# Optimization experiments

Measured on AMD Instinct MI355X. Metric: run time of the kernel, lower is better.

The kernel has to match this reference:

```python
import jax, jax.numpy as jnp
import numpy as np

GAMMA = 0.99
CLIP_VALUE = 5.0
B, T = 4096, 4096


def setup_inputs() -> dict:
    key = jax.random.key(0)
    k1, k2, k3, k4 = jax.random.split(key, 4)
    return {
        "log_probs": jax.random.normal(k1, (B, T), dtype=jnp.float32),
        "logits": jax.random.normal(k2, (B, T), dtype=jnp.float32),
        "weight": jax.random.uniform(k3, (B, T), dtype=jnp.float32),
        "baselines": jax.random.normal(k4, (B, T), dtype=jnp.float32),
    }


def _discounted_reverse_cumsum(wr):
    # wr: [B, T]. c[t] = wr[t] + GAMMA * c[t+1]  (reverse linear recurrence)
    def step(carry, x):
        c = x + GAMMA * carry
        return c, c
    # scan over time, reversed; xs shape [T, B]
    _, cs = jax.lax.scan(step, jnp.zeros(wr.shape[0], wr.dtype), wr.T, reverse=True)
    return cs.T  # [B, T]


def reference(log_probs, logits, weight, baselines):
    rewards = jax.nn.log_sigmoid(logits)                    # [B, T]
    cumulative_rewards = _discounted_reverse_cumsum(weight * rewards)
    advantages = cumulative_rewards - baselines
    advantages = advantages - advantages.mean(axis=0)       # center over batch
    advantages = jnp.clip(advantages, -CLIP_VALUE, CLIP_VALUE)
    generator_objective = (advantages * log_probs).sum(axis=1)  # [B]
    return generator_objective, cumulative_rewards
```

## Files before the change

kernel.cpp:

```cpp
#include <hip/hip_runtime.h>
#include <math.h>

#define B_DIM 4096
#define T_DIM 4096

constexpr float GAMMA_F = 0.99f;
constexpr float CLIP_V  = 5.0f;

constexpr float G2    = GAMMA_F * GAMMA_F;
constexpr float G4    = G2 * G2;
constexpr float G8    = G4 * G4;
constexpr float Q1    = G8 * G8;
constexpr float Q2    = Q1 * Q1;
constexpr float Q4    = Q2 * Q2;
constexpr float Q8    = Q4 * Q4;
constexpr float Q16   = Q8 * Q8;
constexpr float Q32   = Q16 * Q16;
constexpr float G1024 = Q32 * Q32;

__device__ __forceinline__ float pow_g16(int e) {
    float f = 1.0f;
    if (e & 1)  f *= Q1;
    if (e & 2)  f *= Q2;
    if (e & 4)  f *= Q4;
    if (e & 8)  f *= Q8;
    if (e & 16) f *= Q16;
    if (e & 32) f *= Q32;
    return f;
}

__device__ __forceinline__ float lsig(float x) {
    return fminf(x, 0.0f) - __logf(1.0f + __expf(-fabsf(x)));
}

__global__ __launch_bounds__(256) void k_scan(const float4* __restrict__ logits,
                                              const float4* __restrict__ weight,
                                              float4* __restrict__ cum) {
    __shared__ float waveS[4];
    const int row = blockIdx.x;
    const int tid = threadIdx.x;
    const size_t base4 = (size_t)row * (T_DIM / 4) + (size_t)tid * 4;

    float wr[16];
    #pragma unroll
    for (int k = 0; k < 4; ++k) {
        float4 x4 = logits[base4 + k];
        float4 w4 = weight[base4 + k];
        wr[4 * k + 0] = w4.x * lsig(x4.x);
        wr[4 * k + 1] = w4.y * lsig(x4.y);
        wr[4 * k + 2] = w4.z * lsig(x4.z);
        wr[4 * k + 3] = w4.w * lsig(x4.w);
    }

    float V = 0.0f;
    #pragma unroll
    for (int j = 15; j >= 0; --j) V = fmaf(GAMMA_F, V, wr[j]);

    const int wv = tid >> 6, ln = tid & 63;
    float s = V;
    {
        const float F[6] = {Q1, Q2, Q4, Q8, Q16, Q32};
        #pragma unroll
        for (int k = 0; k < 6; ++k) {
            int off = 1 << k;
            float t = __shfl_down(s, off, 64);
            if (ln + off < 64) s = fmaf(F[k], t, s);
        }
    }
    if (ln == 0) waveS[wv] = s;
    __syncthreads();

    float Anext = 0.0f;
    for (int w2 = 3; w2 > wv; --w2) Anext = fmaf(G1024, Anext, waveS[w2]);

    float snext = __shfl_down(s, 1, 64);
    if (ln == 63) snext = 0.0f;
    float carry = fmaf(pow_g16(63 - ln), Anext, snext);

    #pragma unroll
    for (int k = 3; k >= 0; --k) {
        float4 o4;
        o4.w = carry = fmaf(GAMMA_F, carry, wr[4 * k + 3]);
        o4.z = carry = fmaf(GAMMA_F, carry, wr[4 * k + 2]);
        o4.y = carry = fmaf(GAMMA_F, carry, wr[4 * k + 1]);
        o4.x = carry = fmaf(GAMMA_F, carry, wr[4 * k + 0]);
        cum[base4 + k] = o4;
    }
}

__global__ __launch_bounds__(256) void k_zero(float* __restrict__ p) {
    p[blockIdx.x * 256 + threadIdx.x] = 0.0f;
}

__global__ __launch_bounds__(256) void k_colsum(const float* __restrict__ cum,
                                                const float* __restrict__ baselines,
                                                float* __restrict__ colsum) {
    const int t = blockIdx.x * 256 + threadIdx.x;
    size_t p = (size_t)(blockIdx.y * 32) * T_DIM + t;
    float s0 = 0.0f, s1 = 0.0f, s2 = 0.0f, s3 = 0.0f;
    #pragma unroll
    for (int r = 0; r < 32; r += 4) {
        s0 += cum[p] - baselines[p];               p += T_DIM;
        s1 += cum[p] - baselines[p];               p += T_DIM;
        s2 += cum[p] - baselines[p];               p += T_DIM;
        s3 += cum[p] - baselines[p];               p += T_DIM;
    }
    atomicAdd(&colsum[t], (s0 + s1) + (s2 + s3));
}

__global__ __launch_bounds__(256) void k_obj(const float4* __restrict__ cum,
                                             const float4* __restrict__ baselines,
                                             const float4* __restrict__ logp,
                                             const float4* __restrict__ colsum,
                                             float* __restrict__ obj) {
    constexpr float invB = 1.0f / B_DIM;
    const int row = blockIdx.x, tid = threadIdx.x;
    const size_t base4 = (size_t)row * (T_DIM / 4);
    float acc = 0.0f;
    #pragma unroll
    for (int j = 0; j < 4; ++j) {
        int t4 = j * 256 + tid;
        float4 c = cum[base4 + t4];
        float4 b = baselines[base4 + t4];
        float4 l = logp[base4 + t4];
        float4 m = colsum[t4];
        float a0 = fminf(fmaxf(c.x - b.x - m.x * invB, -CLIP_V), CLIP_V);
        float a1 = fminf(fmaxf(c.y - b.y - m.y * invB, -CLIP_V), CLIP_V);
        float a2 = fminf(fmaxf(c.z - b.z - m.z * invB, -CLIP_V), CLIP_V);
        float a3 = fminf(fmaxf(c.w - b.w - m.w * invB, -CLIP_V), CLIP_V);
        acc = fmaf(a0, l.x, acc);
        acc = fmaf(a1, l.y, acc);
        acc = fmaf(a2, l.z, acc);
        acc = fmaf(a3, l.w, acc);
    }
    #pragma unroll
    for (int off = 32; off > 0; off >>= 1) acc += __shfl_down(acc, off, 64);
    __shared__ float ws4[4];
    if ((tid & 63) == 0) ws4[tid >> 6] = acc;
    __syncthreads();
    if (tid == 0) obj[row] = (ws4[0] + ws4[1]) + (ws4[2] + ws4[3]);
}

extern "C" void kernel_launch(void* const* d_in, const int* in_sizes, int n_in,
                              void* d_out, int out_size, void* d_ws, size_t ws_size,
                              hipStream_t stream) {
    const float* log_probs = (const float*)d_in[0];
    const float* logits    = (const float*)d_in[1];
    const float* weight    = (const float*)d_in[2];
    const float* baselines = (const float*)d_in[3];

    float* obj = (float*)d_out;
    float* cum = obj + B_DIM;
    float* colsum = (float*)d_ws;

    k_zero  <<<T_DIM / 256, 256, 0, stream>>>(colsum);
    k_scan  <<<B_DIM, 256, 0, stream>>>((const float4*)logits, (const float4*)weight,
                                        (float4*)cum);
    k_colsum<<<dim3(T_DIM / 256, 128), 256, 0, stream>>>(cum, baselines, colsum);
    k_obj   <<<B_DIM, 256, 0, stream>>>((const float4*)cum, (const float4*)baselines,
                                        (const float4*)log_probs, (const float4*)colsum, obj);
}
```

Before: 277.5 us.

## Coalesce scan loads by interleaving float4 chunks across lanes with per-chunk wave scans

Each thread now owns four float4 chunks strided by 64 across its wave instead of 16 contiguous floats, so global loads and stores are fully coalesced per instruction. To support this, the scan runs four separate wave-level shuffle scans with gamma^4 strides, combines them into a per-wave total, and rebuilds carries per chunk. The aim is better memory access efficiency, paid for with four times as many shuffle operations.

```diff
diff --git a/kernel.cpp b/kernel.cpp
--- a/kernel.cpp
+++ b/kernel.cpp
@@ -18,14 +18,14 @@
 constexpr float Q32   = Q16 * Q16;
 constexpr float G1024 = Q32 * Q32;
 
-__device__ __forceinline__ float pow_g16(int e) {
+__device__ __forceinline__ float pow_g4(int e) {
     float f = 1.0f;
-    if (e & 1)  f *= Q1;
-    if (e & 2)  f *= Q2;
-    if (e & 4)  f *= Q4;
-    if (e & 8)  f *= Q8;
-    if (e & 16) f *= Q16;
-    if (e & 32) f *= Q32;
+    if (e & 1)  f *= G4;
+    if (e & 2)  f *= G8;
+    if (e & 4)  f *= Q1;
+    if (e & 8)  f *= Q2;
+    if (e & 16) f *= Q4;
+    if (e & 32) f *= Q8;
     return f;
 }
 
@@ -39,52 +39,63 @@
     __shared__ float waveS[4];
     const int row = blockIdx.x;
     const int tid = threadIdx.x;
-    const size_t base4 = (size_t)row * (T_DIM / 4) + (size_t)tid * 4;
+    const int wv = tid >> 6, ln = tid & 63;
+    const size_t rb  = (size_t)row * (T_DIM / 4);
+    const int    seg = wv * 256 + ln;
 
     float wr[16];
     #pragma unroll
-    for (int k = 0; k < 4; ++k) {
-        float4 x4 = logits[base4 + k];
-        float4 w4 = weight[base4 + k];
-        wr[4 * k + 0] = w4.x * lsig(x4.x);
-        wr[4 * k + 1] = w4.y * lsig(x4.y);
-        wr[4 * k + 2] = w4.z * lsig(x4.z);
-        wr[4 * k + 3] = w4.w * lsig(x4.w);
+    for (int j = 0; j < 4; ++j) {
+        float4 x4 = logits[rb + seg + j * 64];
+        float4 w4 = weight[rb + seg + j * 64];
+        wr[4 * j + 0] = w4.x * lsig(x4.x);
+        wr[4 * j + 1] = w4.y * lsig(x4.y);
+        wr[4 * j + 2] = w4.z * lsig(x4.z);
+        wr[4 * j + 3] = w4.w * lsig(x4.w);
     }
 
-    float V = 0.0f;
+    float t[4], sn[4];
+    const float F4[6] = {G4, G8, Q1, Q2, Q4, Q8};
     #pragma unroll
-    for (int j = 15; j >= 0; --j) V = fmaf(GAMMA_F, V, wr[j]);
-
-    const int wv = tid >> 6, ln = tid & 63;
-    float s = V;
-    {
-        const float F[6] = {Q1, Q2, Q4, Q8, Q16, Q32};
+    for (int j = 0; j < 4; ++j) {
+        float V = 0.0f;
+        #pragma unroll
+        for (int i = 3; i >= 0; --i) V = fmaf(GAMMA_F, V, wr[4 * j + i]);
+        float s = V;
         #pragma unroll
         for (int k = 0; k < 6; ++k) {
             int off = 1 << k;
-            float t = __shfl_down(s, off, 64);
-            if (ln + off < 64) s = fmaf(F[k], t, s);
+            float u = __shfl_down(s, off, 64);
+            if (ln + off < 64) s = fmaf(F4[k], u, s);
         }
+        float nx = __shfl_down(s, 1, 64);
+        sn[j] = (ln == 63) ? 0.0f : nx;
+        t[j]  = __shfl(s, 0, 64);
     }
-    if (ln == 0) waveS[wv] = s;
+
+    float W = fmaf(Q16, fmaf(Q16, fmaf(Q16, t[3], t[2]), t[1]), t[0]);
+    if (ln == 0) waveS[wv] = W;
     __syncthreads();
 
     float Anext = 0.0f;
     for (int w2 = 3; w2 > wv; --w2) Anext = fmaf(G1024, Anext, waveS[w2]);
 
-    float snext = __shfl_down(s, 1, 64);
-    if (ln == 63) snext = 0.0f;
-    float carry = fmaf(pow_g16(63 - ln), Anext, snext);
+    float U[5];
+    U[4] = Anext;
+    #pragma unroll
+    for (int j = 3; j >= 1; --j) U[j] = fmaf(Q16, U[j + 1], t[j]);
+
+    const float fac = pow_g4(63 - ln);
 
     #pragma unroll
-    for (int k = 3; k >= 0; --k) {
+    for (int j = 0; j < 4; ++j) {
+        float carry = fmaf(fac, U[j + 1], sn[j]);
         float4 o4;
-        o4.w = carry = fmaf(GAMMA_F, carry, wr[4 * k + 3]);
-        o4.z = carry = fmaf(GAMMA_F, carry, wr[4 * k + 2]);
-        o4.y = carry = fmaf(GAMMA_F, carry, wr[4 * k + 1]);
-        o4.x = carry = fmaf(GAMMA_F, carry, wr[4 * k + 0]);
-        cum[base4 + k] = o4;
+        o4.w = carry = fmaf(GAMMA_F, carry, wr[4 * j + 3]);
+        o4.z = carry = fmaf(GAMMA_F, carry, wr[4 * j + 2]);
+        o4.y = carry = fmaf(GAMMA_F, carry, wr[4 * j + 1]);
+        o4.x = carry = fmaf(GAMMA_F, carry, wr[4 * j + 0]);
+        cum[rb + seg + j * 64] = o4;
     }
 }
 
```

New measurement: 281.4 us. About the same (+1.4%).
